# Kernel tuning notes

Hardware: AMD Instinct MI355X
Metric: run time of the kernel (lower is better)

Reference implementation:

```python
import jax, jax.numpy as jnp
import numpy as np

H = 512  # hidden size
E = 512  # embedding / input size
V = 10000  # vocab size


def _lstm_cell(x, h, c, W_ih, W_hh, b_ih, b_hh):
    # torch LSTMCell gate order: i, f, g, o
    gates = x @ W_ih.T + h @ W_hh.T + b_ih + b_hh
    i, f, g, o = jnp.split(gates, 4, axis=-1)
    i = jax.nn.sigmoid(i)
    f = jax.nn.sigmoid(f)
    g = jnp.tanh(g)
    o = jax.nn.sigmoid(o)
    c_new = f * c + i * g
    h_new = o * jnp.tanh(c_new)
    return h_new, c_new


def setup_inputs() -> dict:
    key = jax.random.key(0)
    ks = jax.random.split(key, 14)
    T, B, U = 128, 32, 1024
    s = 0.05
    return {
        "inputs": jax.random.normal(ks[0], (T, B, E), jnp.float32),
        "h0": jax.random.normal(ks[1], (2, B, H), jnp.float32),
        "c0": jax.random.normal(ks[2], (2, B, H), jnp.float32),
        "listener_outputs": jax.random.normal(ks[3], (U, B, H), jnp.float32),
        "W_ih1": jax.random.normal(ks[4], (4 * H, E), jnp.float32) * s,
        "W_hh1": jax.random.normal(ks[5], (4 * H, H), jnp.float32) * s,
        "b_ih1": jax.random.normal(ks[6], (4 * H,), jnp.float32) * s,
        "b_hh1": jax.random.normal(ks[7], (4 * H,), jnp.float32) * s,
        "W_ih2": jax.random.normal(ks[8], (4 * H, H), jnp.float32) * s,
        "W_hh2": jax.random.normal(ks[9], (4 * H, H), jnp.float32) * s,
        "b_ih2": jax.random.normal(ks[10], (4 * H,), jnp.float32) * s,
        "b_hh2": jax.random.normal(ks[11], (4 * H,), jnp.float32) * s,
        "W_out": jax.random.normal(ks[12], (V, H), jnp.float32) * s,
        "b_out": jax.random.normal(ks[13], (V,), jnp.float32) * s,
    }


def reference(inputs, h0, c0, listener_outputs,
              W_ih1, W_hh1, b_ih1, b_hh1,
              W_ih2, W_hh2, b_ih2, b_hh2,
              W_out, b_out):
    # layer-1 LSTMCell + dot-product attention per timestep
    def step1(carry, x_t):
        h1, c1 = carry
        h1, c1 = _lstm_cell(x_t, h1, c1, W_ih1, W_hh1, b_ih1, b_hh1)
        # scores over listener time U: (B, U)
        scores = jnp.einsum('ubh,bh->bu', listener_outputs, h1)
        w = jax.nn.softmax(scores, axis=1)
        ctx = jnp.einsum('ubh,bu->bh', listener_outputs, w)  # (B, H)
        return (h1, c1), ctx

    (_, _), contexts = jax.lax.scan(step1, (h0[0], c0[0]), inputs)  # (T, B, H)

    # layer-2 single-layer LSTM over attention contexts
    def step2(carry, x_t):
        h2, c2 = carry
        h2, c2 = _lstm_cell(x_t, h2, c2, W_ih2, W_hh2, b_ih2, b_hh2)
        return (h2, c2), h2

    (_, _), hs = jax.lax.scan(step2, (h0[1], c0[1]), contexts)  # (T, B, H)

    logits = hs @ W_out.T + b_out  # (T, B, V)
    return jax.nn.softmax(logits, axis=2)
```

## Files before the change

### kernel.cpp

```cpp
#include <hip/hip_runtime.h>

#define T_STEPS 128
#define BATCH   32
#define HID     512
#define EMB     512
#define ULEN    1024
#define VOCAB   10000
#define G4H     2048

#define ARR_STRIDE 16
#define GO_OFF     4096
#define GO_STRIDE  64
#define BAR_WORDS  6144

static inline int cdiv(int a, int b) { return (a + b - 1) / b; }

template <bool TRANSB>
__global__ __launch_bounds__(256)
void gemm_f32(const float* __restrict__ A, long lda, long sA,
              const float* __restrict__ Bm, long ldb, long sB,
              float* __restrict__ C, long ldc, long sC,
              int M, int N, int K, const float* __restrict__ bias)
{
    __shared__ float As[16][68];
    __shared__ float Bs[16][68];
    const int bz = blockIdx.z;
    A  += (size_t)bz * sA;
    Bm += (size_t)bz * sB;
    C  += (size_t)bz * sC;
    const int m0 = blockIdx.y * 64;
    const int n0 = blockIdx.x * 64;
    const int tid = threadIdx.x;
    const int tx = tid & 15, ty = tid >> 4;
    const int lr = tid >> 2;
    const int lk = (tid & 3) * 4;

    float acc[4][4] = {{0.f}};

    for (int k0 = 0; k0 < K; k0 += 16) {
        float4 av = *(const float4*)(A + (size_t)(m0 + lr) * lda + (k0 + lk));
        As[lk + 0][lr] = av.x; As[lk + 1][lr] = av.y;
        As[lk + 2][lr] = av.z; As[lk + 3][lr] = av.w;
        if (TRANSB) {
            const int nr = n0 + lr;
            float4 bv = make_float4(0.f, 0.f, 0.f, 0.f);
            if (nr < N) bv = *(const float4*)(Bm + (size_t)nr * ldb + (k0 + lk));
            Bs[lk + 0][lr] = bv.x; Bs[lk + 1][lr] = bv.y;
            Bs[lk + 2][lr] = bv.z; Bs[lk + 3][lr] = bv.w;
        } else {
            const int kr = tid >> 4;
            const int nc = (tid & 15) * 4;
            float4 bv = make_float4(0.f, 0.f, 0.f, 0.f);
            if (n0 + nc < N) bv = *(const float4*)(Bm + (size_t)(k0 + kr) * ldb + (n0 + nc));
            *(float4*)&Bs[kr][nc] = bv;
        }
        __syncthreads();
#pragma unroll
        for (int kk = 0; kk < 16; ++kk) {
            float ar[4], br[4];
#pragma unroll
            for (int i = 0; i < 4; i++) ar[i] = As[kk][ty * 4 + i];
#pragma unroll
            for (int j = 0; j < 4; j++) br[j] = Bs[kk][tx * 4 + j];
#pragma unroll
            for (int i = 0; i < 4; i++)
#pragma unroll
                for (int j = 0; j < 4; j++)
                    acc[i][j] += ar[i] * br[j];
        }
        __syncthreads();
    }
#pragma unroll
    for (int i = 0; i < 4; i++) {
        const int row = m0 + ty * 4 + i;
#pragma unroll
        for (int j = 0; j < 4; j++) {
            const int col = n0 + tx * 4 + j;
            if (col < N) {
                float v = acc[i][j];
                if (bias) v += bias[col];
                C[(size_t)row * ldc + col] = v;
            }
        }
    }
}

template <bool TRANSB>
__global__ __launch_bounds__(256)
void gemm_f32_big(const float* __restrict__ A, long lda, long sA,
                  const float* __restrict__ Bm, long ldb, long sB,
                  float* __restrict__ C, long ldc, long sC,
                  int M, int N, int K, const float* __restrict__ bias)
{
    __shared__ float As[8][128];
    __shared__ float Bs[8][128];
    const int bz = blockIdx.z;
    A  += (size_t)bz * sA;
    Bm += (size_t)bz * sB;
    C  += (size_t)bz * sC;
    const int m0 = blockIdx.y * 128;
    const int n0 = blockIdx.x * 128;
    const int tid = threadIdx.x;
    const int tx = tid & 15;
    const int ty = tid >> 4;
    const int sr = tid >> 1;
    const int sk = (tid & 1) * 4;

    float acc[2][2][4][4];
#pragma unroll
    for (int ii = 0; ii < 2; ++ii)
#pragma unroll
        for (int jj = 0; jj < 2; ++jj)
#pragma unroll
            for (int i = 0; i < 4; ++i)
#pragma unroll
                for (int j = 0; j < 4; ++j) acc[ii][jj][i][j] = 0.f;

    for (int k0 = 0; k0 < K; k0 += 8) {
        {
            float4 av = *(const float4*)(A + (size_t)(m0 + sr) * lda + (k0 + sk));
            As[sk + 0][sr] = av.x; As[sk + 1][sr] = av.y;
            As[sk + 2][sr] = av.z; As[sk + 3][sr] = av.w;
        }
        if (TRANSB) {
            const int nr = n0 + sr;
            float4 bv = make_float4(0.f, 0.f, 0.f, 0.f);
            if (nr < N) bv = *(const float4*)(Bm + (size_t)nr * ldb + (k0 + sk));
            Bs[sk + 0][sr] = bv.x; Bs[sk + 1][sr] = bv.y;
            Bs[sk + 2][sr] = bv.z; Bs[sk + 3][sr] = bv.w;
        } else {
            const int kr = tid >> 5;
            const int ncc = (tid & 31) * 4;
            float4 bv = make_float4(0.f, 0.f, 0.f, 0.f);
            if (n0 + ncc < N) bv = *(const float4*)(Bm + (size_t)(k0 + kr) * ldb + (n0 + ncc));
            *(float4*)&Bs[kr][ncc] = bv;
        }
        __syncthreads();
#pragma unroll
        for (int kk = 0; kk < 8; ++kk) {
            float4 a0 = *(const float4*)&As[kk][ty * 4];
            float4 a1 = *(const float4*)&As[kk][64 + ty * 4];
            float4 b0 = *(const float4*)&Bs[kk][tx * 4];
            float4 b1 = *(const float4*)&Bs[kk][64 + tx * 4];
            float ar[2][4] = {{a0.x, a0.y, a0.z, a0.w}, {a1.x, a1.y, a1.z, a1.w}};
            float br[2][4] = {{b0.x, b0.y, b0.z, b0.w}, {b1.x, b1.y, b1.z, b1.w}};
#pragma unroll
            for (int ii = 0; ii < 2; ++ii)
#pragma unroll
                for (int jj = 0; jj < 2; ++jj)
#pragma unroll
                    for (int i = 0; i < 4; ++i)
#pragma unroll
                        for (int j = 0; j < 4; ++j)
                            acc[ii][jj][i][j] += ar[ii][i] * br[jj][j];
        }
        __syncthreads();
    }

#pragma unroll
    for (int ii = 0; ii < 2; ++ii)
#pragma unroll
        for (int i = 0; i < 4; ++i) {
            const int row = m0 + ii * 64 + ty * 4 + i;
#pragma unroll
            for (int jj = 0; jj < 2; ++jj) {
                const int cb = n0 + jj * 64 + tx * 4;
                if (cb + 3 < N) {
                    float4 v = make_float4(acc[ii][jj][i][0], acc[ii][jj][i][1],
                                           acc[ii][jj][i][2], acc[ii][jj][i][3]);
                    if (bias) {
                        v.x += bias[cb + 0]; v.y += bias[cb + 1];
                        v.z += bias[cb + 2]; v.w += bias[cb + 3];
                    }
                    *(float4*)(C + (size_t)row * ldc + cb) = v;
                } else {
#pragma unroll
                    for (int j = 0; j < 4; ++j) {
                        const int col = cb + j;
                        if (col < N) {
                            float v = acc[ii][jj][i][j];
                            if (bias) v += bias[col];
                            C[(size_t)row * ldc + col] = v;
                        }
                    }
                }
            }
        }
}

__device__ inline float sigmoidf_(float x) { return 1.f / (1.f + expf(-x)); }

__global__ __launch_bounds__(256, 1)
void lstm_scan(const float* __restrict__ gp,
               const float* __restrict__ Whh,
               const float* __restrict__ h0,
               const float* __restrict__ c0,
               float* __restrict__ h_all,
               unsigned* __restrict__ bar)
{
    __shared__ float h_lds[BATCH * HID];
    __shared__ float w_lds[8 * HID];
    __shared__ float part[256 * 36];
    unsigned* arrive = bar;
    unsigned* go     = bar + GO_OFF;

    const int tid  = threadIdx.x;
    const int bid  = blockIdx.x;
    const int hbase = bid * 2;

    const int ks = tid & 31;
    const int bq = tid >> 5;
    const int kl = ks & 7;

    const int b    = tid >> 3;
    const int nl   = tid & 7;
    const int j    = nl & 1;
    const int lane = tid & 63;
    const int sbase = lane & ~7;
    const int n = ((nl >> 1) << 9) + hbase + j;

#pragma unroll
    for (int i = 0; i < 4; ++i) {
        const int vi = i * 256 + tid;
        const int c  = vi >> 7;
        const int f  = vi & 127;
        const int nd = ((c >> 1) << 9) + hbase + (c & 1);
        float4 v = *(const float4*)(Whh + (size_t)nd * HID + f * 4);
        const int p = f ^ ((f >> 2) & 7);
        *(float4*)&w_lds[(c << 9) + (p << 2)] = v;
    }

    const int sw0 = (((ks * 4 + 0) ^ kl)) << 2;
    const int sw1 = (((ks * 4 + 1) ^ kl)) << 2;
    const int sw2 = (((ks * 4 + 2) ^ kl)) << 2;
    const int sw3 = (((ks * 4 + 3) ^ kl)) << 2;

    float c_state = (nl < 2) ? c0[b * HID + hbase + j] : 0.f;
    float gnext = gp[(size_t)b * G4H + n];

    for (int t = 0; t < T_STEPS; ++t) {
        float gval = gnext;

        const float* hsrc = (t == 0) ? h0 : (h_all + (size_t)(t - 1) * (BATCH * HID));
#pragma unroll
        for (int i = 0; i < 16; ++i) {
            const int vi = i * 256 + tid;
            float4 v = *(const float4*)(hsrc + (size_t)vi * 4);
            const int bb = vi >> 7;
            const int f  = vi & 127;
            const int p  = f ^ ((f >> 2) & 7);
            *(float4*)&h_lds[(bb << 9) + (p << 2)] = v;
        }
        __syncthreads();

        float4 hr[4][4];
#pragma unroll
        for (int rr = 0; rr < 4; ++rr) {
            const int o = (bq * 4 + rr) << 9;
            hr[rr][0] = *(const float4*)(h_lds + o + sw0);
            hr[rr][1] = *(const float4*)(h_lds + o + sw1);
            hr[rr][2] = *(const float4*)(h_lds + o + sw2);
            hr[rr][3] = *(const float4*)(h_lds + o + sw3);
        }

        float acc[32];
#pragma unroll
        for (int c = 0; c < 8; ++c) {
            const int wo = c << 9;
            float4 w0 = *(const float4*)(w_lds + wo + sw0);
            float4 w1 = *(const float4*)(w_lds + wo + sw1);
            float4 w2 = *(const float4*)(w_lds + wo + sw2);
            float4 w3 = *(const float4*)(w_lds + wo + sw3);
#pragma unroll
            for (int rr = 0; rr < 4; ++rr) {
                acc[rr * 8 + c] =
                      (hr[rr][0].x * w0.x + hr[rr][0].y * w0.y
                     + hr[rr][0].z * w0.z + hr[rr][0].w * w0.w)
                    + (hr[rr][1].x * w1.x + hr[rr][1].y * w1.y
                     + hr[rr][1].z * w1.z + hr[rr][1].w * w1.w)
                    + (hr[rr][2].x * w2.x + hr[rr][2].y * w2.y
                     + hr[rr][2].z * w2.z + hr[rr][2].w * w2.w)
                    + (hr[rr][3].x * w3.x + hr[rr][3].y * w3.y
                     + hr[rr][3].z * w3.z + hr[rr][3].w * w3.w);
            }
        }
        {
            float* pw = &part[tid * 36];
#pragma unroll
            for (int i = 0; i < 8; ++i)
                *(float4*)(pw + i * 4) =
                    make_float4(acc[4 * i], acc[4 * i + 1], acc[4 * i + 2], acc[4 * i + 3]);
        }
        __syncthreads();

        float s = gval;
        {
            const float* pr = &part[(b >> 2) * (32 * 36) + (b & 3) * 8 + nl];
#pragma unroll
            for (int kr = 0; kr < 32; ++kr) s += pr[kr * 36];
        }

        float fva = __shfl(s, sbase + 2 + j);
        float gva = __shfl(s, sbase + 4 + j);
        float ova = __shfl(s, sbase + 6 + j);
        if (nl < 2) {
            float iv = sigmoidf_(s);
            float fv = sigmoidf_(fva);
            float gv = tanhf(gva);
            float ov = sigmoidf_(ova);
            c_state = fv * c_state + iv * gv;
            float hn = ov * tanhf(c_state);
            __hip_atomic_store(h_all + ((size_t)t * BATCH + b) * HID + hbase + j,
                               hn, __ATOMIC_RELAXED, __HIP_MEMORY_SCOPE_AGENT);
        }

        {
            const int tn = (t + 1 < T_STEPS) ? (t + 1) : t;
            gnext = gp[((size_t)tn * BATCH + b) * G4H + n];
        }

        __syncthreads();
        const unsigned want = (unsigned)(t + 1);
        if (bid == 0) {
            if (tid == 0)
                __hip_atomic_store(&arrive[0], want, __ATOMIC_RELAXED,
                                   __HIP_MEMORY_SCOPE_AGENT);
            unsigned v;
            do {
                v = __hip_atomic_load(&arrive[tid * ARR_STRIDE], __ATOMIC_RELAXED,
                                      __HIP_MEMORY_SCOPE_AGENT);
            } while (__syncthreads_count(v >= want) < 256);
            if (tid < 32)
                __hip_atomic_store(&go[tid * GO_STRIDE], want, __ATOMIC_RELAXED,
                                   __HIP_MEMORY_SCOPE_AGENT);
        } else if (tid == 0) {
            __hip_atomic_store(&arrive[bid * ARR_STRIDE], want, __ATOMIC_RELAXED,
                               __HIP_MEMORY_SCOPE_AGENT);
            unsigned g;
            do {
                __builtin_amdgcn_s_sleep(1);
                g = __hip_atomic_load(&go[(bid & 31) * GO_STRIDE], __ATOMIC_RELAXED,
                                      __HIP_MEMORY_SCOPE_AGENT);
            } while (g < want);
        }
        __syncthreads();
    }
}

__device__ inline float warpReduceMax_(float v) {
#pragma unroll
    for (int o = 32; o > 0; o >>= 1) v = fmaxf(v, __shfl_xor(v, o));
    return v;
}
__device__ inline float warpReduceSum_(float v) {
#pragma unroll
    for (int o = 32; o > 0; o >>= 1) v += __shfl_xor(v, o);
    return v;
}
__device__ inline float blockReduceMax_(float v, float* red) {
    v = warpReduceMax_(v);
    if ((threadIdx.x & 63) == 0) red[threadIdx.x >> 6] = v;
    __syncthreads();
    float r = fmaxf(fmaxf(red[0], red[1]), fmaxf(red[2], red[3]));
    __syncthreads();
    return r;
}
__device__ inline float blockReduceSum_(float v, float* red) {
    v = warpReduceSum_(v);
    if ((threadIdx.x & 63) == 0) red[threadIdx.x >> 6] = v;
    __syncthreads();
    float r = (red[0] + red[1]) + (red[2] + red[3]);
    __syncthreads();
    return r;
}

__global__ __launch_bounds__(256)
void softmax_u(float* __restrict__ s)
{
    __shared__ float red[4];
    float4* p = (float4*)(s + (size_t)blockIdx.x * ULEN);
    float4 v = p[threadIdx.x];
    float mx = fmaxf(fmaxf(v.x, v.y), fmaxf(v.z, v.w));
    mx = blockReduceMax_(mx, red);
    v.x = expf(v.x - mx); v.y = expf(v.y - mx);
    v.z = expf(v.z - mx); v.w = expf(v.w - mx);
    float sm = blockReduceSum_(v.x + v.y + v.z + v.w, red);
    float inv = 1.f / sm;
    v.x *= inv; v.y *= inv; v.z *= inv; v.w *= inv;
    p[threadIdx.x] = v;
}

__global__ __launch_bounds__(256)
void softmax_v(float* __restrict__ out)
{
    __shared__ float red[4];
    float* p = out + (size_t)blockIdx.x * VOCAB;
    float v[40];
    float mx = -INFINITY;
#pragma unroll
    for (int k = 0; k < 40; ++k) {
        const int i = (k << 8) + (int)threadIdx.x;
        v[k] = (i < VOCAB) ? p[i] : -INFINITY;
        mx = fmaxf(mx, v[k]);
    }
    mx = blockReduceMax_(mx, red);
    float sm = 0.f;
#pragma unroll
    for (int k = 0; k < 40; ++k) {
        v[k] = expf(v[k] - mx);
        sm += v[k];
    }
    sm = blockReduceSum_(sm, red);
    const float inv = 1.f / sm;
#pragma unroll
    for (int k = 0; k < 40; ++k) {
        const int i = (k << 8) + (int)threadIdx.x;
        if (i < VOCAB) p[i] = v[k] * inv;
    }
}

__global__ void prep(const float* __restrict__ bi1, const float* __restrict__ bh1,
                     const float* __restrict__ bi2, const float* __restrict__ bh2,
                     float* __restrict__ bias1, float* __restrict__ bias2,
                     unsigned* __restrict__ flags)
{
    int i = blockIdx.x * 256 + threadIdx.x;
    if (i < G4H) { bias1[i] = bi1[i] + bh1[i]; bias2[i] = bi2[i] + bh2[i]; }
    if (i < 2 * BAR_WORDS) flags[i] = 0u;
}

extern "C" void kernel_launch(void* const* d_in, const int* in_sizes, int n_in,
                              void* d_out, int out_size, void* d_ws, size_t ws_size,
                              hipStream_t stream)
{
    const float* inputs = (const float*)d_in[0];
    const float* h0     = (const float*)d_in[1];
    const float* c0     = (const float*)d_in[2];
    const float* L      = (const float*)d_in[3];
    const float* W_ih1  = (const float*)d_in[4];
    const float* W_hh1  = (const float*)d_in[5];
    const float* b_ih1  = (const float*)d_in[6];
    const float* b_hh1  = (const float*)d_in[7];
    const float* W_ih2  = (const float*)d_in[8];
    const float* W_hh2  = (const float*)d_in[9];
    const float* b_ih2  = (const float*)d_in[10];
    const float* b_hh2  = (const float*)d_in[11];
    const float* W_out  = (const float*)d_in[12];
    const float* b_out  = (const float*)d_in[13];
    float* out = (float*)d_out;

    float* ws    = (float*)d_ws;
    float* gates = ws;
    float* h1    = gates + (size_t)T_STEPS * BATCH * G4H;
    float* h2    = h1    + (size_t)T_STEPS * BATCH * HID;
    float* ctx   = h2    + (size_t)T_STEPS * BATCH * HID;
    float* bias1 = ctx   + (size_t)T_STEPS * BATCH * HID;
    float* bias2 = bias1 + G4H;
    unsigned* flags = (unsigned*)(bias2 + G4H);
    float* scores = gates;

    prep<<<48, 256, 0, stream>>>(b_ih1, b_hh1, b_ih2, b_hh2, bias1, bias2, flags);

    gemm_f32<true><<<dim3(G4H / 64, (T_STEPS * BATCH) / 64, 1), 256, 0, stream>>>(
        inputs, EMB, 0, W_ih1, EMB, 0, gates, G4H, 0,
        T_STEPS * BATCH, G4H, EMB, bias1);

    lstm_scan<<<256, 256, 0, stream>>>(gates, W_hh1, h0, c0, h1, flags);

    gemm_f32<true><<<dim3(ULEN / 64, T_STEPS / 64, BATCH), 256, 0, stream>>>(
        h1, (long)BATCH * HID, HID,
        L,  (long)BATCH * HID, HID,
        scores, (long)BATCH * ULEN, ULEN,
        T_STEPS, ULEN, HID, nullptr);

    softmax_u<<<T_STEPS * BATCH, 256, 0, stream>>>(scores);

    gemm_f32<false><<<dim3(HID / 64, T_STEPS / 64, BATCH), 256, 0, stream>>>(
        scores, (long)BATCH * ULEN, ULEN,
        L,      (long)BATCH * HID,  HID,
        ctx,    (long)BATCH * HID,  HID,
        T_STEPS, HID, ULEN, nullptr);

    gemm_f32<true><<<dim3(G4H / 64, (T_STEPS * BATCH) / 64, 1), 256, 0, stream>>>(
        ctx, HID, 0, W_ih2, HID, 0, gates, G4H, 0,
        T_STEPS * BATCH, G4H, HID, bias2);

    lstm_scan<<<256, 256, 0, stream>>>(gates, W_hh2, h0 + BATCH * HID, c0 + BATCH * HID,
                                       h2, flags + BAR_WORDS);

    gemm_f32_big<true><<<dim3(cdiv(VOCAB, 128), (T_STEPS * BATCH) / 128, 1), 256, 0, stream>>>(
        h2, HID, 0, W_out, HID, 0, out, VOCAB, 0,
        T_STEPS * BATCH, VOCAB, HID, b_out);

    softmax_v<<<T_STEPS * BATCH, 256, 0, stream>>>(out);
}
```

Baseline: 2.555 ms.

## Use split-bf16 MFMA GEMM for output projection instead of fp32 SIMT GEMM

The vocabulary projection GEMM (4096x10000x512) now runs on matrix cores. Both h2 and W_out are split into bf16 hi/lo pairs, and three MFMA passes (hi*hi, hi*lo, lo*hi) recover near-fp32 accuracy. Two conversion kernels are added, and the converted operands are staged in reused workspace buffers (h1 and gates). This trades extra conversion traffic and three passes of matrix work for much higher throughput than the scalar FMA kernel, with a small accuracy risk from dropping the lo*lo term.

Result: faster. 2.253 ms (-11.8%).

```diff
diff --git a/kernel.cpp b/kernel.cpp
--- a/kernel.cpp
+++ b/kernel.cpp
@@ -85,107 +85,117 @@
     }
 }
 
-template <bool TRANSB>
+__device__ inline unsigned short f32_bf16(float x) {
+    unsigned u = __float_as_uint(x);
+    unsigned r = (u + 0x7FFFu + ((u >> 16) & 1u)) >> 16;
+    return (unsigned short)r;
+}
+__device__ inline float bf16_f32(unsigned short h) {
+    return __uint_as_float(((unsigned)h) << 16);
+}
+
 __global__ __launch_bounds__(256)
-void gemm_f32_big(const float* __restrict__ A, long lda, long sA,
-                  const float* __restrict__ Bm, long ldb, long sB,
-                  float* __restrict__ C, long ldc, long sC,
-                  int M, int N, int K, const float* __restrict__ bias)
-{
-    __shared__ float As[8][128];
-    __shared__ float Bs[8][128];
-    const int bz = blockIdx.z;
-    A  += (size_t)bz * sA;
-    Bm += (size_t)bz * sB;
-    C  += (size_t)bz * sC;
+void conv_split(const float* __restrict__ src, unsigned short* __restrict__ dhi,
+                unsigned short* __restrict__ dlo, int n)
+{
+    for (int i = blockIdx.x * 256 + threadIdx.x; i < n; i += gridDim.x * 256) {
+        float a = src[i];
+        unsigned short hi = f32_bf16(a);
+        float r = a - bf16_f32(hi);
+        dhi[i] = hi;
+        dlo[i] = f32_bf16(r);
+    }
+}
+
+typedef __attribute__((ext_vector_type(8))) short bf16x8;
+typedef __attribute__((ext_vector_type(4))) float f32x4;
+
+__global__ __launch_bounds__(256)
+void gemm_bf16s(const unsigned short* __restrict__ Ahi,
+                const unsigned short* __restrict__ Alo,
+                const unsigned short* __restrict__ Bhi,
+                const unsigned short* __restrict__ Blo,
+                float* __restrict__ C, const float* __restrict__ bias,
+                int M, int N, int K)
+{
+    __shared__ unsigned short Asm[128 * 32];
+    __shared__ unsigned short Bsm[128 * 32];
+    const int tid = threadIdx.x;
     const int m0 = blockIdx.y * 128;
     const int n0 = blockIdx.x * 128;
-    const int tid = threadIdx.x;
-    const int tx = tid & 15;
-    const int ty = tid >> 4;
-    const int sr = tid >> 1;
-    const int sk = (tid & 1) * 4;
-
-    float acc[2][2][4][4];
-#pragma unroll
-    for (int ii = 0; ii < 2; ++ii)
-#pragma unroll
-        for (int jj = 0; jj < 2; ++jj)
+    const int w  = tid >> 6;
+    const int l  = tid & 63;
+    const int wr = (w >> 1) * 64;
+    const int wc = (w & 1) * 64;
+    const int fr = l & 15;
+    const int kb = l >> 4;
+
+    f32x4 acc[4][4];
+#pragma unroll
+    for (int i = 0; i < 4; ++i)
+#pragma unroll
+        for (int j = 0; j < 4; ++j) acc[i][j] = (f32x4){0.f, 0.f, 0.f, 0.f};
+
+    const int srow = tid >> 1;
+    const int skh  = (tid & 1) * 16;
+
+#pragma unroll 1
+    for (int pass = 0; pass < 3; ++pass) {
+        const unsigned short* Ap = (pass == 2) ? Alo : Ahi;
+        const unsigned short* Bp = (pass == 1) ? Blo : Bhi;
+#pragma unroll 1
+        for (int kt = 0; kt < K; kt += 32) {
+            {
+                const unsigned short* src = Ap + (size_t)(m0 + srow) * K + kt + skh;
+                float4 v0 = *(const float4*)(src);
+                float4 v1 = *(const float4*)(src + 8);
+                *(float4*)&Asm[srow * 32 + skh] = v0;
+                *(float4*)&Asm[srow * 32 + skh + 8] = v1;
+            }
+            {
+                const int nr = n0 + srow;
+                float4 v0 = make_float4(0.f, 0.f, 0.f, 0.f), v1 = v0;
+                if (nr < N) {
+                    const unsigned short* src = Bp + (size_t)nr * K + kt + skh;
+                    v0 = *(const float4*)(src);
+                    v1 = *(const float4*)(src + 8);
+                }
+                *(float4*)&Bsm[srow * 32 + skh] = v0;
+                *(float4*)&Bsm[srow * 32 + skh + 8] = v1;
+            }
+            __syncthreads();
+            bf16x8 af[4], bf[4];
 #pragma unroll
             for (int i = 0; i < 4; ++i)
-#pragma unroll
-                for (int j = 0; j < 4; ++j) acc[ii][jj][i][j] = 0.f;
-
-    for (int k0 = 0; k0 < K; k0 += 8) {
-        {
-            float4 av = *(const float4*)(A + (size_t)(m0 + sr) * lda + (k0 + sk));
-            As[sk + 0][sr] = av.x; As[sk + 1][sr] = av.y;
-            As[sk + 2][sr] = av.z; As[sk + 3][sr] = av.w;
-        }
-        if (TRANSB) {
-            const int nr = n0 + sr;
-            float4 bv = make_float4(0.f, 0.f, 0.f, 0.f);
-            if (nr < N) bv = *(const float4*)(Bm + (size_t)nr * ldb + (k0 + sk));
-            Bs[sk + 0][sr] = bv.x; Bs[sk + 1][sr] = bv.y;
-            Bs[sk + 2][sr] = bv.z; Bs[sk + 3][sr] = bv.w;
-        } else {
-            const int kr = tid >> 5;
-            const int ncc = (tid & 31) * 4;
-            float4 bv = make_float4(0.f, 0.f, 0.f, 0.f);
-            if (n0 + ncc < N) bv = *(const float4*)(Bm + (size_t)(k0 + kr) * ldb + (n0 + ncc));
-            *(float4*)&Bs[kr][ncc] = bv;
-        }
-        __syncthreads();
-#pragma unroll
-        for (int kk = 0; kk < 8; ++kk) {
-            float4 a0 = *(const float4*)&As[kk][ty * 4];
-            float4 a1 = *(const float4*)&As[kk][64 + ty * 4];
-            float4 b0 = *(const float4*)&Bs[kk][tx * 4];
-            float4 b1 = *(const float4*)&Bs[kk][64 + tx * 4];
-            float ar[2][4] = {{a0.x, a0.y, a0.z, a0.w}, {a1.x, a1.y, a1.z, a1.w}};
-            float br[2][4] = {{b0.x, b0.y, b0.z, b0.w}, {b1.x, b1.y, b1.z, b1.w}};
-#pragma unroll
-            for (int ii = 0; ii < 2; ++ii)
-#pragma unroll
-                for (int jj = 0; jj < 2; ++jj)
-#pragma unroll
-                    for (int i = 0; i < 4; ++i)
-#pragma unroll
-                        for (int j = 0; j < 4; ++j)
-                            acc[ii][jj][i][j] += ar[ii][i] * br[jj][j];
-        }
-        __syncthreads();
-    }
-
-#pragma unroll
-    for (int ii = 0; ii < 2; ++ii)
-#pragma unroll
-        for (int i = 0; i < 4; ++i) {
-            const int row = m0 + ii * 64 + ty * 4 + i;
-#pragma unroll
-            for (int jj = 0; jj < 2; ++jj) {
-                const int cb = n0 + jj * 64 + tx * 4;
-                if (cb + 3 < N) {
-                    float4 v = make_float4(acc[ii][jj][i][0], acc[ii][jj][i][1],
-                                           acc[ii][jj][i][2], acc[ii][jj][i][3]);
-                    if (bias) {
-                        v.x += bias[cb + 0]; v.y += bias[cb + 1];
-                        v.z += bias[cb + 2]; v.w += bias[cb + 3];
-                    }
-                    *(float4*)(C + (size_t)row * ldc + cb) = v;
-                } else {
-#pragma unroll
-                    for (int j = 0; j < 4; ++j) {
-                        const int col = cb + j;
-                        if (col < N) {
-                            float v = acc[ii][jj][i][j];
-                            if (bias) v += bias[col];
-                            C[(size_t)row * ldc + col] = v;
-                        }
-                    }
+                af[i] = *(const bf16x8*)&Asm[(wr + i * 16 + fr) * 32 + kb * 8];
+#pragma unroll
+            for (int j = 0; j < 4; ++j)
+                bf[j] = *(const bf16x8*)&Bsm[(wc + j * 16 + fr) * 32 + kb * 8];
+#pragma unroll
+            for (int i = 0; i < 4; ++i)
+#pragma unroll
+                for (int j = 0; j < 4; ++j)
+                    acc[i][j] = __builtin_amdgcn_mfma_f32_16x16x32_bf16(
+                        af[i], bf[j], acc[i][j], 0, 0, 0);
+            __syncthreads();
+        }
+    }
+
+#pragma unroll
+    for (int i = 0; i < 4; ++i) {
+#pragma unroll
+        for (int j = 0; j < 4; ++j) {
+            const int col = n0 + wc + j * 16 + fr;
+            if (col < N) {
+                const float bv = bias ? bias[col] : 0.f;
+#pragma unroll
+                for (int r = 0; r < 4; ++r) {
+                    const int row = m0 + wr + i * 16 + kb * 4 + r;
+                    C[(size_t)row * N + col] = acc[i][j][r] + bv;
                 }
             }
         }
+    }
 }
 
 __device__ inline float sigmoidf_(float x) { return 1.f / (1.f + expf(-x)); }
@@ -459,11 +469,17 @@
     unsigned* flags = (unsigned*)(bias2 + G4H);
     float* scores = gates;
 
+    const int MA = T_STEPS * BATCH;
+    unsigned short* ahi = (unsigned short*)h1;
+    unsigned short* alo = ahi + (size_t)MA * HID;
+    unsigned short* bhi = (unsigned short*)gates;
+    unsigned short* blo = bhi + (size_t)VOCAB * HID;
+
     prep<<<48, 256, 0, stream>>>(b_ih1, b_hh1, b_ih2, b_hh2, bias1, bias2, flags);
 
-    gemm_f32<true><<<dim3(G4H / 64, (T_STEPS * BATCH) / 64, 1), 256, 0, stream>>>(
+    gemm_f32<true><<<dim3(G4H / 64, MA / 64, 1), 256, 0, stream>>>(
         inputs, EMB, 0, W_ih1, EMB, 0, gates, G4H, 0,
-        T_STEPS * BATCH, G4H, EMB, bias1);
+        MA, G4H, EMB, bias1);
 
     lstm_scan<<<256, 256, 0, stream>>>(gates, W_hh1, h0, c0, h1, flags);
 
@@ -481,16 +497,18 @@
         ctx,    (long)BATCH * HID,  HID,
         T_STEPS, HID, ULEN, nullptr);
 
-    gemm_f32<true><<<dim3(G4H / 64, (T_STEPS * BATCH) / 64, 1), 256, 0, stream>>>(
+    gemm_f32<true><<<dim3(G4H / 64, MA / 64, 1), 256, 0, stream>>>(
         ctx, HID, 0, W_ih2, HID, 0, gates, G4H, 0,
-        T_STEPS * BATCH, G4H, HID, bias2);
+        MA, G4H, HID, bias2);
 
     lstm_scan<<<256, 256, 0, stream>>>(gates, W_hh2, h0 + BATCH * HID, c0 + BATCH * HID,
                                        h2, flags + BAR_WORDS);
 
-    gemm_f32_big<true><<<dim3(cdiv(VOCAB, 128), (T_STEPS * BATCH) / 128, 1), 256, 0, stream>>>(
-        h2, HID, 0, W_out, HID, 0, out, VOCAB, 0,
-        T_STEPS * BATCH, VOCAB, HID, b_out);
+    conv_split<<<2048, 256, 0, stream>>>(W_out, bhi, blo, VOCAB * HID);
+    conv_split<<<2048, 256, 0, stream>>>(h2, ahi, alo, MA * HID);
+
+    gemm_bf16s<<<dim3(cdiv(VOCAB, 128), MA / 128, 1), 256, 0, stream>>>(
+        ahi, alo, bhi, blo, out, b_out, MA, VOCAB, HID);
 
     softmax_v<<<T_STEPS * BATCH, 256, 0, stream>>>(out);
 }
```
